# Kernel tuning notes

Measured on AMD Instinct MI355X. Metric: run time of the kernel, lower is better.

Reference implementation:

```python
import jax, jax.numpy as jnp
import numpy as np

N_QUBITS = 12
N_LAYERS = 3
HID = 16
IN_DIM = 6
BATCH = 4096
C64 = jnp.complex64


def _ry(t):
    c = jnp.cos(t / 2).astype(C64)
    s = jnp.sin(t / 2).astype(C64)
    return jnp.stack([jnp.stack([c, -s], -1), jnp.stack([s, c], -1)], -2)


def _rx(t):
    c = jnp.cos(t / 2).astype(C64)
    s = jnp.sin(t / 2).astype(C64)
    js = 1j * s
    return jnp.stack([jnp.stack([c, -js], -1), jnp.stack([-js, c], -1)], -2)


def _rz(t):
    e = jnp.exp(-1j * t.astype(C64) / 2)
    z = jnp.zeros_like(e)
    return jnp.stack([jnp.stack([e, z], -1), jnp.stack([z, jnp.conj(e)], -1)], -2)


def _apply_1q(state, U, wire):
    # state: (B,) + (2,)*n ; U: (2,2) shared or (B,2,2) per-sample
    s = jnp.moveaxis(state, wire + 1, 1)
    if U.ndim == 2:
        s = jnp.einsum('ij,bj...->bi...', U, s)
    else:
        s = jnp.einsum('bij,bj...->bi...', U, s)
    return jnp.moveaxis(s, 1, wire + 1)


def _cnot(state, c, t):
    ax_c = c + 1
    s0 = jnp.take(state, 0, axis=ax_c)
    s1 = jnp.take(state, 1, axis=ax_c)
    t_ax = t + 1 if t < c else t  # target axis after removing control axis
    s1 = jnp.flip(s1, axis=t_ax)  # X on target when control=1
    return jnp.stack([s0, s1], axis=ax_c)


def _quantum(angles, qparams):
    # angles: (B, n_qubits) angle-encoding RY rotations; qparams: (L, n, 3)
    B = angles.shape[0]
    n = N_QUBITS
    state = jnp.zeros((B,) + (2,) * n, C64).at[(slice(None),) + (0,) * n].set(1.0)
    for i in range(n):
        state = _apply_1q(state, _ry(angles[:, i]), i)
    for l in range(N_LAYERS):
        for i in range(n):
            # RX then RY then RZ on wire i -> fused 2x2
            U = _rz(qparams[l, i, 2]) @ _ry(qparams[l, i, 1]) @ _rx(qparams[l, i, 0])
            state = _apply_1q(state, U, i)
        for i in range(n - 1):
            state = _cnot(state, i, i + 1)
        if n > 2:
            state = _cnot(state, n - 1, 0)
    p = state.real ** 2 + state.imag ** 2  # (B,) + (2,)*n
    evs = []
    for i in range(n):
        axes = tuple(a for a in range(1, n + 1) if a != i + 1)
        pi = p.sum(axes)  # (B, 2)
        evs.append(pi[:, 0] - pi[:, 1])
    return jnp.stack(evs, axis=1)  # (B, n) PauliZ expvals


def setup_inputs() -> dict:
    key = jax.random.key(0)
    ks = jax.random.split(key, 14)
    w = lambda k, shape: jax.random.normal(k, shape, jnp.float32) * 0.1
    return {
        'x': jax.random.normal(ks[0], (BATCH, IN_DIM), jnp.float32),
        'W1': w(ks[1], (HID, IN_DIM)), 'b1': w(ks[2], (HID,)),
        'W2': w(ks[3], (HID, HID)), 'b2': w(ks[4], (HID,)),
        'W3': w(ks[5], (N_QUBITS, HID)), 'b3': w(ks[6], (N_QUBITS,)),
        'qparams': w(ks[7], (N_LAYERS, N_QUBITS, 3)),
        'P1': w(ks[8], (HID, N_QUBITS)), 'c1': w(ks[9], (HID,)),
        'P2': w(ks[10], (8, HID)), 'c2': w(ks[11], (8,)),
        'P3': w(ks[12], (1, 8)), 'c3': w(ks[13], (1,)),
    }


def reference(x, W1, b1, W2, b2, W3, b3, qparams, P1, c1, P2, c2, P3, c3):
    # classical preprocessor (dropout = identity at inference)
    h = jax.nn.relu(x @ W1.T + b1)
    h = jax.nn.relu(h @ W2.T + b2)
    angles = h @ W3.T + b3  # (B, n_qubits)
    q = _quantum(angles, qparams)  # (B, n_qubits)
    # classical postprocessor
    o = jax.nn.relu(q @ P1.T + c1)
    o = jax.nn.relu(o @ P2.T + c2)
    o = jax.nn.sigmoid(o @ P3.T + c3)
    return o.squeeze(-1)  # (B,)
```

## Files before the change

kernel.cpp:

```cpp
#include <hip/hip_runtime.h>
#include <stdint.h>

#define NQ   12
#define DIM  4096
#define TPB  256

typedef float   v2f   __attribute__((ext_vector_type(2)));
typedef float   v4f   __attribute__((ext_vector_type(4)));
typedef float   f32x4 __attribute__((ext_vector_type(4)));
typedef _Float16 v2h  __attribute__((ext_vector_type(2)));
typedef _Float16 f16x8 __attribute__((ext_vector_type(8)));
typedef uint32_t u32x4 __attribute__((ext_vector_type(4)));


constexpr int par(uint32_t x) { return __builtin_popcount(x) & 1; }
constexpr int chbit(uint32_t x) { int b=-1; for (int i=0;i<32;++i) if ((x>>i)&1u) b=i; return b; }

constexpr void bmm(uint32_t* C, const uint32_t* A, const uint32_t* B) {
  for (int i = 0; i < NQ; ++i) {
    uint32_t r = 0;
    for (int j = 0; j < NQ; ++j) if ((A[i] >> j) & 1u) r ^= B[j];
    C[i] = r;
  }
}
constexpr void binv(const uint32_t* M, uint32_t* Inv) {
  uint32_t A[NQ] = {}, I[NQ] = {};
  for (int i = 0; i < NQ; ++i) { A[i] = M[i]; I[i] = 1u << i; }
  for (int c = 0; c < NQ; ++c) {
    int piv = -1;
    for (int r = c; r < NQ; ++r) if ((A[r] >> c) & 1u) { piv = r; break; }
    if (piv < 0) continue;
    uint32_t ta = A[c]; A[c] = A[piv]; A[piv] = ta;
    uint32_t ti = I[c]; I[c] = I[piv]; I[piv] = ti;
    for (int r = 0; r < NQ; ++r)
      if (r != c && ((A[r] >> c) & 1u)) { A[r] ^= A[c]; I[r] ^= I[c]; }
  }
  for (int i = 0; i < NQ; ++i) Inv[i] = I[i];
}

constexpr void pass_vm(int p, uint32_t* v, uint32_t* m) {
  uint32_t A[NQ] = {}; A[0] = 0xFFEu;
  for (int i = 1; i < NQ; ++i) A[i] = (1u << (i + 1)) - 1u;
  uint32_t A2[NQ] = {}, Ai[NQ] = {}, A2i[NQ] = {};
  bmm(A2, A, A); binv(A, Ai); binv(A2, A2i);
  const uint32_t* M  = (p < 3) ? A  : A2;
  const uint32_t* Mi = (p < 3) ? Ai : A2i;
  const int wb = (p % 3) * 4;
  for (int i = 0; i < 4; ++i) {
    uint32_t col = 0;
    for (int r = 0; r < NQ; ++r) col |= ((Mi[r] >> (wb + i)) & 1u) << r;
    v[i] = col; m[i] = M[wb + i];
  }
}

constexpr bool addvec(uint32_t* red, uint32_t x) {
  while (x) {
    const int h = chbit(x);
    if (red[h]) x ^= red[h]; else { red[h] = x; return true; }
  }
  return false;
}
constexpr int rankbits(const uint32_t* w, int n) {
  uint32_t red[8] = {}; int r = 0;
  for (int q = 0; q < n; ++q) {
    uint32_t x = w[q];
    while (x) {
      const int h = chbit(x);
      if (red[h]) x ^= red[h]; else { red[h] = x; ++r; break; }
    }
  }
  return r;
}
constexpr void perm_decode(int idx, int* s) {
  int avail[6] = {0, 1, 2, 3, 4, 5};
  const int f[6] = {120, 24, 6, 2, 1, 1};
  for (int i = 0; i < 6; ++i) {
    const int k = idx / f[i]; idx %= f[i];
    s[i] = avail[k];
    for (int j = k; j < 5 - i; ++j) avail[j] = avail[j + 1];
  }
}

struct Lay { uint32_t d[12]; uint32_t mi[12]; int tok; };

constexpr Lay make_lay(int p, const Lay& prev, bool hasPrev) {
  Lay L{};
  uint32_t v[4] = {}, m[4] = {};
  pass_vm(p, v, m);
  L.d[0] = v[0]; L.d[1] = v[1]; L.d[6] = v[2]; L.d[7] = v[3];
  uint32_t red[16] = {};
  addvec(red, v[0]); addvec(red, v[1]); addvec(red, v[2]); addvec(red, v[3]);
  L.tok = 0;
  if (p < 5) {
    uint32_t vn[4] = {}, mn[4] = {};
    pass_vm(p + 1, vn, mn);
    bool roles0 = true;
    for (int i = 0; i < 4; ++i)
      if (par(m[i] & vn[0]) || par(m[i] & vn[1])) roles0 = false;
    if (roles0) {
      uint32_t tmp[16] = {};
      for (int i = 0; i < 16; ++i) tmp[i] = red[i];
      if (addvec(tmp, vn[0]) && addvec(tmp, vn[1])) {
        addvec(red, vn[0]); addvec(red, vn[1]);
        L.d[8] = vn[0]; L.d[9] = vn[1]; L.tok = 1;
      }
    }
  }
  uint32_t pool[8] = {}; int np = 0;
  const int need = L.tok ? 6 : 8;
  for (int b = 0; b < 12 && np < need; ++b) {
    uint32_t cand = 1u << b;
    for (int i = 0; i < 4; ++i) if ((m[i] >> b) & 1u) cand ^= v[i];
    if (addvec(red, cand)) pool[np++] = cand;
  }
  if (!L.tok) { L.d[8] = pool[6]; L.d[9] = pool[7]; }
  const int S[6] = {2, 3, 4, 5, 10, 11};
  for (int i = 0; i < 6; ++i) L.d[S[i]] = pool[i];
  uint32_t Mr[NQ] = {}, miC[NQ] = {};
  for (int i = 0; i < NQ; ++i) {
    uint32_t r = 0;
    for (int j = 0; j < NQ; ++j) r |= ((L.d[j] >> i) & 1u) << j;
    Mr[i] = r;
  }
  binv(Mr, miC);
  uint32_t V[8] = {}; int nv = 0; int mode5 = 1;
  if (!hasPrev) {
    for (int k = 0; k < 8; ++k) {
      uint32_t c = 0;
      for (int bb = 0; bb < 12; ++bb) c |= (uint32_t)par(miC[bb] & (1u << k)) << bb;
      V[nv++] = c;
    }
    mode5 = 1;
  } else {
    const uint32_t src[6] = {prev.d[2], prev.d[3], prev.d[4], prev.d[5],
                             prev.d[1], prev.d[6]};
    for (int k = 0; k < 6; ++k) {
      uint32_t c = 0;
      for (int bb = 0; bb < 12; ++bb) c |= (uint32_t)par(miC[bb] & src[k]) << bb;
      V[nv++] = c;
    }
    mode5 = prev.tok ? 0 : 1;
  }
  int bestP = 0, bestSc = -1;
  for (int pi = 0; pi < 720; ++pi) {
    int sg[6] = {}; perm_decode(pi, sg);
    uint32_t pw[8] = {};
    for (int k = 0; k < nv; ++k) {
      uint32_t w = 0;
      if (mode5) {
        w |= V[k] & 3u;
        for (int i = 0; i < 3; ++i)
          w |= (uint32_t)((V[k] >> S[sg[i]]) & 1u) << (2 + i);
      } else {
        for (int i = 0; i < 3; ++i)
          w |= (uint32_t)((V[k] >> S[sg[i]]) & 1u) << i;
      }
      pw[k] = w;
    }
    const int sc = rankbits(pw, nv);
    if (sc > bestSc) { bestSc = sc; bestP = pi; }
  }
  int sg[6] = {}; perm_decode(bestP, sg);
  for (int i = 0; i < 6; ++i) L.d[S[i]] = pool[sg[i]];
  for (int i = 0; i < NQ; ++i) {
    uint32_t r = 0;
    for (int j = 0; j < NQ; ++j) r |= ((L.d[j] >> i) & 1u) << j;
    Mr[i] = r;
  }
  binv(Mr, L.mi);
  return L;
}

constexpr Lay LY0 = make_lay(0, Lay{}, false);
constexpr Lay LY1 = make_lay(1, LY0, true);
constexpr Lay LY2 = make_lay(2, LY1, true);
constexpr Lay LY3 = make_lay(3, LY2, true);
constexpr Lay LY4 = make_lay(4, LY3, true);
constexpr Lay LY5 = make_lay(5, LY4, true);

constexpr uint32_t imgL(const Lay& l, uint32_t y) {
  uint32_t r = 0;
  for (int b = 0; b < 12; ++b) r |= (uint32_t)par(l.mi[b] & y) << b;
  return r;
}

struct PCon {
  uint32_t WN[4], WQ1, WQ2, WW0, WW1;
  uint32_t WV0, WV3;
  uint32_t WT0, WT1;
  int      W4;
  uint32_t SM[12], robin[12];
  uint8_t  layer, wb;
};

constexpr PCon make_pcon(const Lay& lp, const Lay& ln, int p) {
  PCon c{};
  c.layer = (uint8_t)((p < 3) ? 1 : 2); c.wb = (uint8_t)((p % 3) * 4);
  for (int k = 0; k < 4; ++k) c.WN[k] = imgL(ln, lp.d[2 + k]);
  c.WQ1 = imgL(ln, lp.d[1]);  c.WQ2 = imgL(ln, lp.d[6]);
  c.WW0 = imgL(ln, lp.d[10]); c.WW1 = imgL(ln, lp.d[11]);
  c.WV0 = imgL(ln, lp.d[0]);  c.WV3 = imgL(ln, lp.d[7]);
  c.WT0 = imgL(ln, lp.d[8]);  c.WT1 = imgL(ln, lp.d[9]);
  c.W4 = (lp.tok && c.WT0 == 1u && c.WT1 == 2u) ? 1 : 0;
  return c;
}
constexpr PCon make_pcon5(const Lay& lp) {
  PCon c{};
  c.layer = 2; c.wb = 8; c.W4 = 0;
  uint32_t A[NQ] = {}; A[0] = 0xFFEu;
  for (int i = 1; i < NQ; ++i) A[i] = (1u << (i + 1)) - 1u;
  uint32_t A2[NQ] = {}, A3[NQ] = {};
  bmm(A2, A, A); bmm(A3, A2, A);
  for (int i = 0; i < NQ; ++i) {
    uint32_t sm = 0;
    sm |= (uint32_t)par(A3[i] & lp.d[2])  << 0;
    sm |= (uint32_t)par(A3[i] & lp.d[3])  << 1;
    sm |= (uint32_t)par(A3[i] & lp.d[4])  << 2;
    sm |= (uint32_t)par(A3[i] & lp.d[5])  << 3;
    sm |= (uint32_t)par(A3[i] & lp.d[1])  << 4;
    sm |= (uint32_t)par(A3[i] & lp.d[6])  << 5;
    sm |= (uint32_t)par(A3[i] & lp.d[10]) << 6;
    sm |= (uint32_t)par(A3[i] & lp.d[11]) << 7;
    c.SM[i] = sm;
    c.robin[i] = (uint32_t)par(A3[i] & lp.d[0])
               | (uint32_t)par(A3[i] & lp.d[7]) << 1
               | (uint32_t)par(A3[i] & lp.d[8]) << 2
               | (uint32_t)par(A3[i] & lp.d[9]) << 3;
  }
  return c;
}

constexpr PCon PC0 = make_pcon(LY0, LY1, 0);
constexpr PCon PC1 = make_pcon(LY1, LY2, 1);
constexpr PCon PC2 = make_pcon(LY2, LY3, 2);
constexpr PCon PC3 = make_pcon(LY3, LY4, 3);
constexpr PCon PC4 = make_pcon(LY4, LY5, 4);
constexpr PCon PC5 = make_pcon5(LY5);

template<int P> constexpr PCon pget() {
  if constexpr (P == 0) return PC0;
  else if constexpr (P == 1) return PC1;
  else if constexpr (P == 2) return PC2;
  else if constexpr (P == 3) return PC3;
  else if constexpr (P == 4) return PC4;
  else return PC5;
}

struct InitC { uint32_t ICt[8]; uint32_t ICj[16]; };
constexpr InitC make_init() {
  InitC ic{};
  for (int b = 0; b < 8; ++b) ic.ICt[b] = imgL(LY0, 1u << b);
  uint32_t Jc[4] = {};
  for (int b = 0; b < 4; ++b) Jc[b] = imgL(LY0, 1u << (8 + b));
  for (int j = 0; j < 16; ++j) {
    uint32_t r = 0;
    for (int b = 0; b < 4; ++b) if ((j >> b) & 1) r ^= Jc[b];
    ic.ICj[j] = r;
  }
  return ic;
}
constexpr InitC IC = make_init();

__device__ __forceinline__ v2f cmulf(v2f a, v2f b) {
  return (v2f){a.x * b.x - a.y * b.y, a.x * b.y + a.y * b.x};
}
__device__ __forceinline__ uint32_t f2h2(float a, float b) {
  return __builtin_bit_cast(uint32_t, __builtin_amdgcn_cvt_pkrtz(a, b));
}
__device__ __forceinline__ uint32_t pk_rtn(float a, float b) {
  v2h h = {(_Float16)a, (_Float16)b};
  return __builtin_bit_cast(uint32_t, h);
}
__device__ __forceinline__ void build_u(const float* __restrict__ qp, int l, int w, float U[8]) {
  float p0 = qp[(l * 12 + w) * 3 + 0];
  float p1 = qp[(l * 12 + w) * 3 + 1];
  float p2 = qp[(l * 12 + w) * 3 + 2];
  float cx, sx, cy, sy, cz, sz;
  sincosf(0.5f * p0, &sx, &cx);
  sincosf(0.5f * p1, &sy, &cy);
  sincosf(0.5f * p2, &sz, &cz);
  float M00x =  cy * cx, M00y =  sy * sx;
  float M01x = -sy * cx, M01y = -cy * sx;
  float M10x =  sy * cx, M10y = -cy * sx;
  float M11x =  cy * cx, M11y = -sy * sx;
  U[0] = cz * M00x + sz * M00y; U[1] = cz * M00y - sz * M00x;
  U[2] = cz * M01x + sz * M01y; U[3] = cz * M01y - sz * M01x;
  U[4] = cz * M10x - sz * M10y; U[5] = cz * M10y + sz * M10x;
  U[6] = cz * M11x - sz * M11y; U[7] = cz * M11y + sz * M11x;
}
__device__ __forceinline__ int am_col(int c, int i) {
  return ((((c >> 2) ^ ((i >> 1) & 3)) << 2) | (c & 3));
}

template<int P>
__device__ __forceinline__ void build_am_g(uint32_t* __restrict__ Am_g,
                                           const v2f (*gg)[12][4], int t) {
  constexpr PCon pc = pget<P>();
  const int r_ = t >> 4, c_ = t & 15;
  v2f e = (v2f){1.f, 0.f};
  #pragma unroll
  for (int i = 0; i < 4; ++i) {
    v2f u = gg[pc.layer - 1][pc.wb + i][(((r_ >> i) & 1) << 1) | ((c_ >> i) & 1)];
    e = cmulf(e, u);
  }
  const int ra = 2 * r_, rb = 2 * r_ + 1;
  Am_g[P * 512 + ra * 16 + am_col(c_, ra)] = pk_rtn(e.x, -e.y);
  Am_g[P * 512 + rb * 16 + am_col(c_, rb)] = pk_rtn(e.y, e.x);
}

__global__ __launch_bounds__(256) void prep_kernel(const float* __restrict__ qp,
                                                   uint32_t* __restrict__ Am_g,
                                                   float* __restrict__ U0_g) {
  __shared__ v2f gg[2][12][4];
  const int t = threadIdx.x;
  if (t < 24) {
    const int L = t / 12 + 1, w = t % 12;
    float U[8]; build_u(qp, L, w, U);
    gg[L - 1][w][0] = (v2f){U[0], U[1]};
    gg[L - 1][w][1] = (v2f){U[2], U[3]};
    gg[L - 1][w][2] = (v2f){U[4], U[5]};
    gg[L - 1][w][3] = (v2f){U[6], U[7]};
  } else if (t >= 32 && t < 44) {
    const int w = t - 32;
    float U[8]; build_u(qp, 0, w, U);
    #pragma unroll
    for (int k = 0; k < 8; ++k) U0_g[w * 8 + k] = U[k];
  }
  __syncthreads();
  build_am_g<0>(Am_g, gg, t);
  build_am_g<1>(Am_g, gg, t);
  build_am_g<2>(Am_g, gg, t);
  build_am_g<3>(Am_g, gg, t);
  build_am_g<4>(Am_g, gg, t);
  build_am_g<5>(Am_g, gg, t);
}

template<int P, bool LAST>
__device__ __forceinline__ void do_pass(uint32_t* st, f16x8 a0, f16x8 a1,
                                        int lane, int wvl, float* ev) {
  constexpr PCon pc = pget<P>();
  const int n = lane & 15, q = lane >> 4;
  const int rb = (n << 2) | (q << 6) | (wvl << 10);
  int wb_ = 0;
  if constexpr (!LAST) {
    wb_ = ((n & 1) ? pc.WN[0] : 0) ^ ((n & 2) ? pc.WN[1] : 0)
        ^ ((n & 4) ? pc.WN[2] : 0) ^ ((n & 8) ? pc.WN[3] : 0)
        ^ ((q & 1) ? pc.WQ1 : 0)   ^ ((q & 2) ? pc.WQ2 : 0)
        ^ ((wvl & 1) ? pc.WW0 : 0) ^ ((wvl & 2) ? pc.WW1 : 0);
  }
  const f32x4 z = {0.f, 0.f, 0.f, 0.f};
  if constexpr (!LAST && pc.W4) {
    uint32_t wbuf[4][4];
    #pragma unroll
    for (int T = 0; T < 4; ++T) {
      u32x4 braw = *reinterpret_cast<const u32x4*>(&st[rb ^ (T << 8)]);
      f16x8 bf = __builtin_bit_cast(f16x8, braw);
      f32x4 c0 = __builtin_amdgcn_mfma_f32_16x16x32_f16(a0, bf, z, 0, 0, 0);
      f32x4 c1 = __builtin_amdgcn_mfma_f32_16x16x32_f16(a1, bf, z, 0, 0, 0);
      wbuf[0][T] = f2h2(c0.x, c0.y);
      wbuf[1][T] = f2h2(c0.z, c0.w);
      wbuf[2][T] = f2h2(c1.x, c1.y);
      wbuf[3][T] = f2h2(c1.z, c1.w);
    }
    #pragma unroll
    for (int c = 0; c < 4; ++c) {
      const int A = wb_ ^ ((c & 1) ? pc.WV0 : 0) ^ ((c & 2) ? pc.WV3 : 0);
      const bool s0 = A & 1, s1 = A & 2;
      uint32_t x0 = wbuf[c][0], x1 = wbuf[c][1], x2 = wbuf[c][2], x3 = wbuf[c][3];
      uint32_t y0 = s0 ? x1 : x0, y1 = s0 ? x0 : x1;
      uint32_t y2 = s0 ? x3 : x2, y3 = s0 ? x2 : x3;
      uint32_t z0 = s1 ? y2 : y0, z1 = s1 ? y3 : y1;
      uint32_t z2 = s1 ? y0 : y2, z3 = s1 ? y1 : y3;
      *reinterpret_cast<u32x4*>(&st[A & ~3]) = (u32x4){z0, z1, z2, z3};
    }
  } else if constexpr (!LAST) {
    #pragma unroll
    for (int T = 0; T < 4; ++T) {
      u32x4 braw = *reinterpret_cast<const u32x4*>(&st[rb ^ (T << 8)]);
      f16x8 bf = __builtin_bit_cast(f16x8, braw);
      f32x4 c0 = __builtin_amdgcn_mfma_f32_16x16x32_f16(a0, bf, z, 0, 0, 0);
      f32x4 c1 = __builtin_amdgcn_mfma_f32_16x16x32_f16(a1, bf, z, 0, 0, 0);
      const int A = wb_ ^ ((T & 1) ? pc.WT0 : 0) ^ ((T & 2) ? pc.WT1 : 0);
      st[A]                      = f2h2(c0.x, c0.y);
      st[A ^ pc.WV0]             = f2h2(c0.z, c0.w);
      st[A ^ pc.WV3]             = f2h2(c1.x, c1.y);
      st[A ^ (pc.WV0 ^ pc.WV3)]  = f2h2(c1.z, c1.w);
    }
  } else {
    float pr[16];
    #pragma unroll
    for (int T = 0; T < 4; ++T) {
      u32x4 braw = *reinterpret_cast<const u32x4*>(&st[rb ^ (T << 8)]);
      f16x8 bf = __builtin_bit_cast(f16x8, braw);
      f32x4 c0 = __builtin_amdgcn_mfma_f32_16x16x32_f16(a0, bf, z, 0, 0, 0);
      f32x4 c1 = __builtin_amdgcn_mfma_f32_16x16x32_f16(a1, bf, z, 0, 0, 0);
      const int nb = ((T & 1) << 2) | ((T >> 1) << 3);
      pr[nb]     = c0.x * c0.x + c0.y * c0.y;
      pr[nb | 1] = c0.z * c0.z + c0.w * c0.w;
      pr[nb | 2] = c1.x * c1.x + c1.y * c1.y;
      pr[nb | 3] = c1.z * c1.z + c1.w * c1.w;
    }
    #pragma unroll
    for (int gs = 1; gs < 16; gs <<= 1) {
      #pragma unroll
      for (int j = 0; j < 16; ++j) {
        if (j & gs) continue;
        float u = pr[j], w2 = pr[j | gs];
        pr[j] = u + w2; pr[j | gs] = u - w2;
      }
    }
    const int pw = n | (q << 4) | (wvl << 6);
    #pragma unroll
    for (int i = 0; i < NQ; ++i) {
      float h = pr[pc.robin[i]];
      int s = (__popc((int)pc.SM[i] & pw) & 1) << 31;
      ev[i] = __int_as_float(__float_as_int(h) ^ s);
    }
  }
}

#define LDA(P, A0, A1) {                                                        \
  const int li_ = lane & 15;                                                    \
  const int q_  = (lane >> 4) ^ ((li_ >> 1) & 3);                               \
  A0 = __builtin_bit_cast(f16x8,                                                \
      *reinterpret_cast<const u32x4*>(Am_g + (P) * 512 + li_ * 16 + q_ * 4));   \
  A1 = __builtin_bit_cast(f16x8,                                                \
      *reinterpret_cast<const u32x4*>(Am_g + (P) * 512 + (li_ + 16) * 16 + q_ * 4)); \
}

__global__ __launch_bounds__(TPB, 8) void hqc_kernel(
    const float* __restrict__ x,  const float* __restrict__ W1, const float* __restrict__ b1,
    const float* __restrict__ W2, const float* __restrict__ b2,
    const float* __restrict__ W3, const float* __restrict__ b3,
    const float* __restrict__ P1, const float* __restrict__ c1,
    const float* __restrict__ P2, const float* __restrict__ c2,
    const float* __restrict__ P3, const float* __restrict__ c3,
    const uint32_t* __restrict__ Am_g, const float* __restrict__ U0_g,
    float* __restrict__ out)
{
  __shared__ __align__(16) uint32_t st[DIM];
  __shared__ v4f  gpk0[12][2];
  __shared__ float red[4][NQ];

  const int s    = blockIdx.x;
  const int t    = threadIdx.x;
  const int lane = t & 63;
  const int wv   = t >> 6;

  f16x8 a0c, a1c, a0n, a1n;
  LDA(0, a0c, a1c)

  if (wv == 0 && lane < 16) {
    float a = b1[lane];
    #pragma unroll
    for (int k = 0; k < 6; ++k) a = fmaf(W1[lane * 6 + k], x[s * 6 + k], a);
    float h1 = fmaxf(a, 0.f);
    float a2 = b2[lane];
    #pragma unroll
    for (int k = 0; k < 16; ++k) a2 = fmaf(W2[lane * 16 + k], __shfl(h1, k, 64), a2);
    float h2 = fmaxf(a2, 0.f);
    const int lw = (lane < NQ) ? lane : 0;
    float a3 = b3[lw];
    #pragma unroll
    for (int k = 0; k < 16; ++k) a3 = fmaf(W3[lw * 16 + k], __shfl(h2, k, 64), a3);
    if (lane < NQ) {
      const float* u = U0_g + lane * 8;
      float ca, sa; sincosf(0.5f * a3, &sa, &ca);
      float c0x = u[0] * ca + u[2] * sa, c0y = u[1] * ca + u[3] * sa;
      float c1x = u[4] * ca + u[6] * sa, c1y = u[5] * ca + u[7] * sa;
      gpk0[lane][0] = (v4f){c0x, c0x, -c0y, c0y};
      gpk0[lane][1] = (v4f){c1x, c1x, -c1y, c1y};
    }
  }
  __syncthreads();

  {
    int tb = 0;
    #pragma unroll
    for (int b = 0; b < 8; ++b) if ((t >> b) & 1) tb ^= IC.ICt[b];
    v2f acc = (v2f){1.f, 0.f};
    #pragma unroll
    for (int i = 0; i < 8; ++i) {
      v4f gk = gpk0[i][(t >> i) & 1];
      acc = gk.xy * acc + gk.zw * acc.yx;
    }
    v2f l16[16];
    l16[0] = acc;
    #pragma unroll
    for (int i = 0; i < 4; ++i) {
      v4f g0 = gpk0[8 + i][0], g1 = gpk0[8 + i][1];
      #pragma unroll
      for (int j = 0; j < (1 << i); ++j) {
        v2f a = l16[j];
        l16[j | (1 << i)] = g1.xy * a + g1.zw * a.yx;
        l16[j]            = g0.xy * a + g0.zw * a.yx;
      }
    }
    #pragma unroll
    for (int j = 0; j < 16; ++j) st[tb ^ IC.ICj[j]] = f2h2(l16[j].x, l16[j].y);
  }
  __syncthreads();

  float ev[NQ];
  LDA(1, a0n, a1n)
  do_pass<0, false>(st, a0c, a1c, lane, wv, ev); __syncthreads();
  a0c = a0n; a1c = a1n; LDA(2, a0n, a1n)
  do_pass<1, false>(st, a0c, a1c, lane, wv, ev); __syncthreads();
  a0c = a0n; a1c = a1n; LDA(3, a0n, a1n)
  do_pass<2, false>(st, a0c, a1c, lane, wv, ev); __syncthreads();
  a0c = a0n; a1c = a1n; LDA(4, a0n, a1n)
  do_pass<3, false>(st, a0c, a1c, lane, wv, ev); __syncthreads();
  a0c = a0n; a1c = a1n; LDA(5, a0n, a1n)
  do_pass<4, false>(st, a0c, a1c, lane, wv, ev); __syncthreads();
  a0c = a0n; a1c = a1n;
  do_pass<5, true >(st, a0c, a1c, lane, wv, ev);

  #pragma unroll
  for (int off = 32; off >= 1; off >>= 1) {
    #pragma unroll
    for (int i = 0; i < NQ; ++i) ev[i] += __shfl_xor(ev[i], off, 64);
  }
  if (lane == 0) {
    #pragma unroll
    for (int i = 0; i < NQ; ++i) red[wv][i] = ev[i];
  }
  __syncthreads();

  if (wv == 0 && lane < 16) {
    float q = (lane < NQ)
      ? (red[0][lane] + red[1][lane] + red[2][lane] + red[3][lane])
      : 0.f;
    float a = c1[lane];
    #pragma unroll
    for (int j = 0; j < NQ; ++j) a = fmaf(P1[lane * NQ + j], __shfl(q, j, 64), a);
    float o1 = fmaxf(a, 0.f);
    float a2 = c2[lane & 7];
    #pragma unroll
    for (int j = 0; j < 16; ++j) a2 = fmaf(P2[(lane & 7) * 16 + j], __shfl(o1, j, 64), a2);
    float o2 = fmaxf(a2, 0.f);
    float a3 = c3[0];
    #pragma unroll
    for (int j = 0; j < 8; ++j) a3 = fmaf(P3[j], __shfl(o2, j, 64), a3);
    if (lane == 0) out[s] = 1.f / (1.f + expf(-a3));
  }
}

extern "C" void kernel_launch(void* const* d_in, const int* in_sizes, int n_in,
                              void* d_out, int out_size, void* d_ws, size_t ws_size,
                              hipStream_t stream) {
  (void)in_sizes; (void)n_in; (void)ws_size;
  uint32_t* Am_g = (uint32_t*)d_ws;
  float*    U0_g = (float*)((char*)d_ws + 6 * 512 * 4);
  const float* qp = (const float*)d_in[7];
  prep_kernel<<<1, 256, 0, stream>>>(qp, Am_g, U0_g);
  hqc_kernel<<<out_size, TPB, 0, stream>>>(
      (const float*)d_in[0],  (const float*)d_in[1],  (const float*)d_in[2],
      (const float*)d_in[3],  (const float*)d_in[4],  (const float*)d_in[5],
      (const float*)d_in[6],
      (const float*)d_in[8],  (const float*)d_in[9],
      (const float*)d_in[10], (const float*)d_in[11],
      (const float*)d_in[12], (const float*)d_in[13],
      Am_g, U0_g,
      (float*)d_out);
}
```

Baseline: 48.89 us.

## Search qubit-to-address layouts enabling unswizzled 128-bit LDS stores between passes

Extends the compile-time layout search so that, when a pass emits two token bits, it prefers basis vectors whose low address bits do not depend on the next pass's mask bits. It also runs a separate permutation search for a rank-3 mapping. The W4 wide-store path is enabled only when every write offset keeps its low two bits clear. That makes each 4-element group contiguous and aligned, so the per-lane select/swizzle before the 128-bit LDS store can be dropped. The aim is fewer LDS write instructions and fewer VALU selects, at the cost of more constexpr search and a stricter gate that may enable W4 for fewer passes.

Result: slower. 55.40 us (+13.3%).

```diff
diff --git a/kernel.cpp b/kernel.cpp
--- a/kernel.cpp
+++ b/kernel.cpp
@@ -81,7 +81,7 @@
   }
 }
 
-struct Lay { uint32_t d[12]; uint32_t mi[12]; int tok; };
+struct Lay { uint32_t d[12]; uint32_t mi[12]; int tok; int lowf; int rank3; };
 
 constexpr Lay make_lay(int p, const Lay& prev, bool hasPrev) {
   Lay L{};
@@ -90,10 +90,12 @@
   L.d[0] = v[0]; L.d[1] = v[1]; L.d[6] = v[2]; L.d[7] = v[3];
   uint32_t red[16] = {};
   addvec(red, v[0]); addvec(red, v[1]); addvec(red, v[2]); addvec(red, v[3]);
-  L.tok = 0;
+  L.tok = 0; L.lowf = 0; L.rank3 = 0;
+  uint32_t mn0 = 0, mn1 = 0;
   if (p < 5) {
     uint32_t vn[4] = {}, mn[4] = {};
     pass_vm(p + 1, vn, mn);
+    mn0 = mn[0]; mn1 = mn[1];
     bool roles0 = true;
     for (int i = 0; i < 4; ++i)
       if (par(m[i] & vn[0]) || par(m[i] & vn[1])) roles0 = false;
@@ -106,12 +108,42 @@
       }
     }
   }
+  const int need = L.tok ? 6 : 8;
   uint32_t pool[8] = {}; int np = 0;
-  const int need = L.tok ? 6 : 8;
-  for (int b = 0; b < 12 && np < need; ++b) {
-    uint32_t cand = 1u << b;
-    for (int i = 0; i < 4; ++i) if ((m[i] >> b) & 1u) cand ^= v[i];
-    if (addvec(red, cand)) pool[np++] = cand;
+  if (L.tok) {
+    uint32_t red2[16] = {};
+    for (int i = 0; i < 16; ++i) red2[i] = red[i];
+    uint32_t p2[8] = {}; int n2 = 0;
+    for (int b = 0; b < 12 && n2 < need; ++b) {
+      uint32_t cand = 1u << b;
+      for (int i = 0; i < 4; ++i) if ((m[i] >> b) & 1u) cand ^= v[i];
+      if (par(cand & mn0) || par(cand & mn1)) continue;
+      if (addvec(red2, cand)) p2[n2++] = cand;
+    }
+    for (int a = 0; a < 12 && n2 < need; ++a)
+      for (int b = a + 1; b < 12 && n2 < need; ++b) {
+        uint32_t ca = 1u << a, cb = 1u << b;
+        for (int i = 0; i < 4; ++i) {
+          if ((m[i] >> a) & 1u) ca ^= v[i];
+          if ((m[i] >> b) & 1u) cb ^= v[i];
+        }
+        uint32_t cand = ca ^ cb;
+        if (par(cand & mn0) || par(cand & mn1)) continue;
+        if (addvec(red2, cand)) p2[n2++] = cand;
+      }
+    if (n2 == need) {
+      L.lowf = 1;
+      for (int i = 0; i < need; ++i) pool[i] = p2[i];
+      np = need;
+      for (int i = 0; i < 16; ++i) red[i] = red2[i];
+    }
+  }
+  if (np < need) {
+    for (int b = 0; b < 12 && np < need; ++b) {
+      uint32_t cand = 1u << b;
+      for (int i = 0; i < 4; ++i) if ((m[i] >> b) & 1u) cand ^= v[i];
+      if (addvec(red, cand)) pool[np++] = cand;
+    }
   }
   if (!L.tok) { L.d[8] = pool[6]; L.d[9] = pool[7]; }
   const int S[6] = {2, 3, 4, 5, 10, 11};
@@ -123,14 +155,13 @@
     Mr[i] = r;
   }
   binv(Mr, miC);
-  uint32_t V[8] = {}; int nv = 0; int mode5 = 1;
+  uint32_t V[8] = {}; int nv = 0;
   if (!hasPrev) {
     for (int k = 0; k < 8; ++k) {
       uint32_t c = 0;
       for (int bb = 0; bb < 12; ++bb) c |= (uint32_t)par(miC[bb] & (1u << k)) << bb;
       V[nv++] = c;
     }
-    mode5 = 1;
   } else {
     const uint32_t src[6] = {prev.d[2], prev.d[3], prev.d[4], prev.d[5],
                              prev.d[1], prev.d[6]};
@@ -139,26 +170,40 @@
       for (int bb = 0; bb < 12; ++bb) c |= (uint32_t)par(miC[bb] & src[k]) << bb;
       V[nv++] = c;
     }
-    mode5 = prev.tok ? 0 : 1;
+  }
+  bool wantB128 = false;
+  if (hasPrev && prev.tok && prev.lowf) {
+    if (!par(m[0] & prev.d[0]) && !par(m[1] & prev.d[0]) &&
+        !par(m[0] & prev.d[7]) && !par(m[1] & prev.d[7])) wantB128 = true;
   }
   int bestP = 0, bestSc = -1;
-  for (int pi = 0; pi < 720; ++pi) {
-    int sg[6] = {}; perm_decode(pi, sg);
-    uint32_t pw[8] = {};
-    for (int k = 0; k < nv; ++k) {
-      uint32_t w = 0;
-      if (mode5) {
-        w |= V[k] & 3u;
-        for (int i = 0; i < 3; ++i)
-          w |= (uint32_t)((V[k] >> S[sg[i]]) & 1u) << (2 + i);
-      } else {
-        for (int i = 0; i < 3; ++i)
-          w |= (uint32_t)((V[k] >> S[sg[i]]) & 1u) << i;
+  if (wantB128) {
+    for (int pi = 0; pi < 720; ++pi) {
+      int sg[6] = {}; perm_decode(pi, sg);
+      uint32_t pw[8] = {};
+      for (int k = 0; k < nv; ++k) {
+        uint32_t w = 0;
+        for (int i = 0; i < 3; ++i) w |= (uint32_t)((V[k] >> S[sg[i]]) & 1u) << i;
+        pw[k] = w;
       }
-      pw[k] = w;
-    }
-    const int sc = rankbits(pw, nv);
-    if (sc > bestSc) { bestSc = sc; bestP = pi; }
+      const int sc = rankbits(pw, nv);
+      if (sc > bestSc) { bestSc = sc; bestP = pi; }
+    }
+    if (bestSc >= 3) L.rank3 = 1;
+  }
+  if (!L.rank3) {
+    bestP = 0; bestSc = -1;
+    for (int pi = 0; pi < 720; ++pi) {
+      int sg[6] = {}; perm_decode(pi, sg);
+      uint32_t pw[8] = {};
+      for (int k = 0; k < nv; ++k) {
+        uint32_t w = V[k] & 3u;
+        for (int i = 0; i < 3; ++i) w |= (uint32_t)((V[k] >> S[sg[i]]) & 1u) << (2 + i);
+        pw[k] = w;
+      }
+      const int sc = rankbits(pw, nv);
+      if (sc > bestSc) { bestSc = sc; bestP = pi; }
+    }
   }
   int sg[6] = {}; perm_decode(bestP, sg);
   for (int i = 0; i < 6; ++i) L.d[S[i]] = pool[sg[i]];
@@ -201,7 +246,10 @@
   c.WW0 = imgL(ln, lp.d[10]); c.WW1 = imgL(ln, lp.d[11]);
   c.WV0 = imgL(ln, lp.d[0]);  c.WV3 = imgL(ln, lp.d[7]);
   c.WT0 = imgL(ln, lp.d[8]);  c.WT1 = imgL(ln, lp.d[9]);
-  c.W4 = (lp.tok && c.WT0 == 1u && c.WT1 == 2u) ? 1 : 0;
+  const bool low = (((c.WN[0] | c.WN[1] | c.WN[2] | c.WN[3] |
+                      c.WQ1 | c.WQ2 | c.WW0 | c.WW1 |
+                      c.WV0 | c.WV3) & 3u) == 0);
+  c.W4 = (lp.tok && c.WT0 == 1u && c.WT1 == 2u && low && ln.rank3) ? 1 : 0;
   return c;
 }
 constexpr PCon make_pcon5(const Lay& lp) {
@@ -365,13 +413,8 @@
     #pragma unroll
     for (int c = 0; c < 4; ++c) {
       const int A = wb_ ^ ((c & 1) ? pc.WV0 : 0) ^ ((c & 2) ? pc.WV3 : 0);
-      const bool s0 = A & 1, s1 = A & 2;
-      uint32_t x0 = wbuf[c][0], x1 = wbuf[c][1], x2 = wbuf[c][2], x3 = wbuf[c][3];
-      uint32_t y0 = s0 ? x1 : x0, y1 = s0 ? x0 : x1;
-      uint32_t y2 = s0 ? x3 : x2, y3 = s0 ? x2 : x3;
-      uint32_t z0 = s1 ? y2 : y0, z1 = s1 ? y3 : y1;
-      uint32_t z2 = s1 ? y0 : y2, z3 = s1 ? y1 : y3;
-      *reinterpret_cast<u32x4*>(&st[A & ~3]) = (u32x4){z0, z1, z2, z3};
+      *reinterpret_cast<u32x4*>(&st[A]) =
+          (u32x4){wbuf[c][0], wbuf[c][1], wbuf[c][2], wbuf[c][3]};
     }
   } else if constexpr (!LAST) {
     #pragma unroll
```
